# Kernel optimization log

Measured on AMD Instinct MI355X. Metric: run time of the kernel, lower is better.

The kernel has to match this reference:

```python
import jax, jax.numpy as jnp
import numpy as np

N1, N2 = 25000, 25000
N = N1 + N2
E = 800000
D1, D2 = 2000, 500
P = 128        # proj_dim
H, C = 4, 32   # heads, hidden_channels (H*C == 128)
NEG_SLOPE = 0.2


def glorot(key, shape):
    fan_in, fan_out = shape[0], shape[-1]
    s = jnp.sqrt(6.0 / (fan_in + fan_out))
    return jax.random.uniform(key, shape, jnp.float32, -s, s)


def setup_inputs() -> dict:
    key = jax.random.key(0)
    ks = jax.random.split(key, 12)
    return {
        "x_mrna": jax.random.normal(ks[0], (N1, D1), jnp.float32),
        "x_mirna": jax.random.normal(ks[1], (N2, D2), jnp.float32),
        "Wp1": glorot(ks[2], (D1, P)),
        "bp1": jnp.zeros((P,), jnp.float32),
        "Wp2": glorot(ks[3], (D2, P)),
        "bp2": jnp.zeros((P,), jnp.float32),
        "Wl": glorot(ks[4], (P, H * C)),   # GATv2 lin_l (source)
        "Wr": glorot(ks[5], (P, H * C)),   # GATv2 lin_r (target)
        "att": glorot(ks[6], (H, C)),       # GATv2 attention vector a
        "b_gat": jnp.zeros((H * C,), jnp.float32),
        "edge_index": jax.random.randint(ks[7], (2, E), 0, N, jnp.int32),
    }


def gatv2_conv(x, edge_index, Wl, Wr, att, b_gat):
    # x: [N, P] -> out: [N, H*C]; PyG GATv2Conv, add_self_loops=False, concat=True
    src, dst = edge_index[0], edge_index[1]
    xl = (x @ Wl).reshape(N, H, C)  # source-side transform
    xr = (x @ Wr).reshape(N, H, C)  # target-side transform
    # per-edge attention logits: a . LeakyReLU(xl[src] + xr[dst])  -> [E, H]
    g = jax.nn.leaky_relu(xl[src] + xr[dst], NEG_SLOPE)
    e = jnp.einsum('ehc,hc->eh', g, att)
    # softmax over incoming edges per destination node, per head
    m = jax.ops.segment_max(e, dst, num_segments=N)          # [N, H]
    ex = jnp.exp(e - m[dst])                                  # [E, H]
    denom = jax.ops.segment_sum(ex, dst, num_segments=N)     # [N, H]
    alpha = ex / (denom[dst] + 1e-16)                         # [E, H]
    msg = alpha[:, :, None] * xl[src]                         # [E, H, C]
    out = jax.ops.segment_sum(msg, dst, num_segments=N)      # [N, H, C]
    return out.reshape(N, H * C) + b_gat


def reference(x_mrna, x_mirna, Wp1, bp1, Wp2, bp2, Wl, Wr, att, b_gat, edge_index):
    # per-omic projection to shared proj_dim, then stack into one node set
    h1 = x_mrna @ Wp1 + bp1
    h2 = x_mirna @ Wp2 + bp2
    x = jnp.concatenate([h1, h2], axis=0)  # [N, P]
    out = gatv2_conv(x, edge_index, Wl, Wr, att, b_gat)
    return jax.nn.elu(out)
```

## Files before the change

### kernel.cpp

```cpp
#include <hip/hip_runtime.h>

#define NN 50000
#define NE 800000
#define PD 128
#define NBLK 196
#define GB1 391
#define M_HALF 25000

typedef __attribute__((ext_vector_type(8))) short bf16x8;
typedef __attribute__((ext_vector_type(4))) float f32x4;

__device__ __forceinline__ float bf2f(unsigned short h) {
  union { unsigned u; float f; } v; v.u = ((unsigned)h) << 16; return v.f;
}
__device__ __forceinline__ unsigned short f2bf(float f) {
  union { float f; unsigned u; } v; v.f = f;
  unsigned r = (v.u + 0x7FFFu + ((v.u >> 16) & 1u)) >> 16;
  return (unsigned short)r;
}
__device__ __forceinline__ unsigned pack2(float a, float b) {
  return (unsigned)f2bf(a) | ((unsigned)f2bf(b) << 16);
}

__global__ __launch_bounds__(256) void wtrans(
    const float* __restrict__ Wp1, const float* __restrict__ Wp2,
    const float* __restrict__ Wl, const float* __restrict__ Wr,
    const float* __restrict__ bp1, const float* __restrict__ bp2,
    unsigned short* __restrict__ Wct1, unsigned short* __restrict__ Wct2,
    float* __restrict__ biasc) {
  int b = blockIdx.x, n = threadIdx.x;
  __shared__ float arow[128];
  const float* W = (n < 128) ? Wl : Wr;
  int nc = n & 127;
  if (b < 2560) {
    int is1 = (b < 2048) ? 1 : 0;
    int k = is1 ? b : (b - 2048);
    int Kv = is1 ? 2000 : 500;
    unsigned short v = 0;
    if (k < Kv) {
      if (n < 128) arow[n] = is1 ? Wp1[k * 128 + n] : Wp2[k * 128 + n];
      __syncthreads();
      float s = 0.f;
      for (int p = 0; p < 128; ++p) s += arow[p] * W[p * 128 + nc];
      v = f2bf(s);
    }
    int ch = k >> 5, kq = (k >> 3) & 3, e = k & 7;
    size_t idx = (size_t)ch * 8192 + (size_t)(n * 4 + (kq ^ ((n >> 1) & 3))) * 8 + e;
    if (is1) Wct1[idx] = v; else Wct2[idx] = v;
  } else {
    float s1 = 0.f, s2 = 0.f;
    for (int p = 0; p < 128; ++p) {
      float w = W[p * 128 + nc];
      s1 += bp1[p] * w;
      s2 += bp2[p] * w;
    }
    biasc[n] = s1;
    biasc[256 + n] = s2;
  }
}

__global__ __launch_bounds__(256) void big_gemm(
    const float* __restrict__ x1, const float* __restrict__ x2,
    const unsigned short* __restrict__ Wct1, const unsigned short* __restrict__ Wct2,
    const float* __restrict__ biasc,
    unsigned short* __restrict__ XLb, float* __restrict__ XR) {
  __shared__ __align__(64) unsigned short lds[2 * 10752];
  int tid = threadIdx.x;
  int wave = tid >> 6, lane = tid & 63;
  int m16 = lane & 15, quad = lane >> 4;

  int inp = (blockIdx.x >= GB1) ? 1 : 0;
  int blk = inp ? (blockIdx.x - GB1) : blockIdx.x;
  const float* A = inp ? x2 : x1;
  const unsigned short* Wct = inp ? Wct2 : Wct1;
  const int K = inp ? 500 : 2000;
  const int nch = inp ? 16 : 63;
  int row0 = blk * 64;

  int ar = tid >> 2, ako = (tid & 3) << 3;
  bool arow_ok = (row0 + ar) < M_HALF;
  const float* aptr = A + (size_t)(row0 + ar) * K + ako;

  int swz = (quad ^ ((m16 >> 1) & 3)) << 3;
  int boffA[4], boffB[4];
#pragma unroll
  for (int i = 0; i < 4; ++i) boffA[i] = (i * 16 + m16) * 40 + quad * 8;
#pragma unroll
  for (int j = 0; j < 4; ++j) boffB[j] = (wave * 64 + j * 16 + m16) * 32 + swz;

  f32x4 acc[4][4];
#pragma unroll
  for (int i = 0; i < 4; ++i)
#pragma unroll
    for (int j = 0; j < 4; ++j) acc[i][j] = (f32x4){0.f, 0.f, 0.f, 0.f};

  float4 pa0, pa1;

#define GLB(ch, buf)                                                          \
  {                                                                           \
    const unsigned short* wp_ = Wct + (size_t)(ch) * 8192;                    \
    unsigned short* bb_ = lds + (buf) * 10752 + 2560;                         \
    _Pragma("unroll") for (int ii = 0; ii < 4; ++ii) {                        \
      int gb_ = (ii * 4 + wave) * 64;                                         \
      __builtin_amdgcn_global_load_lds(                                       \
          (const __attribute__((address_space(1))) void*)(wp_ +               \
              (size_t)(gb_ + lane) * 8),                                      \
          (__attribute__((address_space(3))) void*)(bb_ + (size_t)gb_ * 8),   \
          16, 0, 0);                                                          \
    }                                                                         \
  }

#define LOADA(ch)                                                             \
  {                                                                           \
    int k0_ = (ch) * 32;                                                      \
    if (arow_ok) {                                                            \
      pa0 = *(const float4*)(aptr + k0_);                                     \
      pa1 = *(const float4*)(aptr + k0_ + 4);                                 \
    }                                                                         \
  }

#define STOREA(buf)                                                           \
  {                                                                           \
    unsigned short* As_ = lds + (buf) * 10752;                                \
    uint4 wA;                                                                 \
    if (arow_ok) {                                                            \
      wA.x = pack2(pa0.x, pa0.y); wA.y = pack2(pa0.z, pa0.w);                 \
      wA.z = pack2(pa1.x, pa1.y); wA.w = pack2(pa1.z, pa1.w);                 \
    } else { wA.x = wA.y = wA.z = wA.w = 0u; }                                \
    *(uint4*)(As_ + ar * 40 + ako) = wA;                                      \
  }

  GLB(0, 0);
  LOADA(0);
  STOREA(0);
  __syncthreads();

  for (int ch = 0; ch < nch; ++ch) {
    int cur = ch & 1;
    if (ch + 1 < nch) { GLB(ch + 1, cur ^ 1); LOADA(ch + 1); }
    {
      const unsigned short* As_ = lds + cur * 10752;
      const unsigned short* Bs_ = As_ + 2560;
      bf16x8 a[4], b[4];
#pragma unroll
      for (int i = 0; i < 4; ++i) a[i] = *(const bf16x8*)(As_ + boffA[i]);
#pragma unroll
      for (int j = 0; j < 4; ++j) b[j] = *(const bf16x8*)(Bs_ + boffB[j]);
#pragma unroll
      for (int i = 0; i < 4; ++i)
#pragma unroll
        for (int j = 0; j < 4; ++j)
          acc[i][j] =
              __builtin_amdgcn_mfma_f32_16x16x32_bf16(a[i], b[j], acc[i][j], 0, 0, 0);
    }
    if (ch + 1 < nch) STOREA(cur ^ 1);
    __syncthreads();
  }

  const float* bc = biasc + inp * 256;
#pragma unroll
  for (int i = 0; i < 4; ++i) {
    int rb = row0 + i * 16 + quad * 4;
#pragma unroll
    for (int j = 0; j < 4; ++j) {
      int c = wave * 64 + j * 16 + m16;
      float bv = bc[c];
#pragma unroll
      for (int r = 0; r < 4; ++r) {
        if (rb + r < M_HALF) {
          size_t grow = (size_t)inp * M_HALF + rb + r;
          float v = acc[i][j][r] + bv;
          if (c < PD) XLb[grow * PD + c] = f2bf(v);
          else XR[grow * PD + (c - PD)] = v;
        }
      }
    }
  }
#undef GLB
#undef LOADA
#undef STOREA
}

__global__ __launch_bounds__(256) void zero_deg(int* __restrict__ deg) {
  int i = blockIdx.x * 256 + threadIdx.x;
  if (i < NN) deg[i] = 0;
}

__global__ __launch_bounds__(256) void hist(const int* __restrict__ edge,
                                            int* __restrict__ deg) {
  int i = blockIdx.x * 256 + threadIdx.x;
  if (i < NE) atomicAdd(&deg[edge[NE + i]], 1);
}

__global__ __launch_bounds__(256) void scan1(const int* __restrict__ deg,
                                             int* __restrict__ bsum) {
  __shared__ int sd[256];
  int i = blockIdx.x * 256 + threadIdx.x;
  sd[threadIdx.x] = (i < NN) ? deg[i] : 0;
  __syncthreads();
  for (int off = 128; off > 0; off >>= 1) {
    if (threadIdx.x < off) sd[threadIdx.x] += sd[threadIdx.x + off];
    __syncthreads();
  }
  if (threadIdx.x == 0) bsum[blockIdx.x] = sd[0];
}

__global__ __launch_bounds__(64) void scan2(const int* __restrict__ bsum,
                                            int* __restrict__ boff) {
  if (threadIdx.x == 0) {
    int run = 0;
    for (int b = 0; b < NBLK; ++b) { boff[b] = run; run += bsum[b]; }
  }
}

__global__ __launch_bounds__(256) void scan3(const int* __restrict__ deg,
                                             const int* __restrict__ boff,
                                             int* __restrict__ start,
                                             int* __restrict__ cursor) {
  __shared__ int sd[256];
  int i = blockIdx.x * 256 + threadIdx.x;
  int v = (i < NN) ? deg[i] : 0;
  sd[threadIdx.x] = v;
  __syncthreads();
  for (int off = 1; off < 256; off <<= 1) {
    int t = (threadIdx.x >= off) ? sd[threadIdx.x - off] : 0;
    __syncthreads();
    sd[threadIdx.x] += t;
    __syncthreads();
  }
  if (i < NN) {
    int excl = boff[blockIdx.x] + sd[threadIdx.x] - v;
    start[i] = excl;
    cursor[i] = excl;
  }
  if (blockIdx.x == 0 && threadIdx.x == 0) start[NN] = NE;
}

__global__ __launch_bounds__(256) void scatter(const int* __restrict__ edge,
                                               int* __restrict__ cursor,
                                               int* __restrict__ esrc) {
  int i = blockIdx.x * 256 + threadIdx.x;
  if (i < NE) {
    int dst = edge[NE + i];
    int pos = atomicAdd(&cursor[dst], 1);
    esrc[pos] = edge[i];
  }
}

__global__ __launch_bounds__(256) void gat_fused(
    const unsigned short* __restrict__ XLb, const float* __restrict__ XR,
    const float* __restrict__ att, const float* __restrict__ bg,
    const int* __restrict__ start, const int* __restrict__ esrc,
    float* __restrict__ out) {
  int wave = threadIdx.x >> 6, lane = threadIdx.x & 63;
  int d = blockIdx.x * 4 + wave;
  int f0 = lane * 2;

  float2 xr = *(const float2*)(XR + (size_t)d * PD + f0);
  float a0c = att[f0], a1c = att[f0 + 1];

  int s = start[d], e_end = start[d + 1];

  float m = -INFINITY, l = 0.f, acc0 = 0.f, acc1 = 0.f;
  for (int j = s; j < e_end; ++j) {
    int src = esrc[j];
    unsigned xlu = *(const unsigned*)(XLb + (size_t)src * PD + f0);
    float xl0 = bf2f((unsigned short)(xlu & 0xFFFFu));
    float xl1 = bf2f((unsigned short)(xlu >> 16));
    float z0 = xl0 + xr.x, z1 = xl1 + xr.y;
    float g0 = z0 > 0.f ? z0 : 0.2f * z0;
    float g1 = z1 > 0.f ? z1 : 0.2f * z1;
    float t = a0c * g0 + a1c * g1;
    t += __shfl_xor(t, 1);
    t += __shfl_xor(t, 2);
    t += __shfl_xor(t, 4);
    t += __shfl_xor(t, 8);
    float mn = fmaxf(m, t);
    float c = __expf(m - mn);
    float p = __expf(t - mn);
    l = l * c + p;
    acc0 = acc0 * c + p * xl0;
    acc1 = acc1 * c + p * xl1;
    m = mn;
  }

  float inv = 1.f / (l + 1e-16f);
  float v0 = acc0 * inv + bg[f0];
  float v1 = acc1 * inv + bg[f0 + 1];
  v0 = v0 > 0.f ? v0 : expm1f(v0);
  v1 = v1 > 0.f ? v1 : expm1f(v1);
  *(float2*)(out + (size_t)d * PD + f0) = make_float2(v0, v1);
}

extern "C" void kernel_launch(void* const* d_in, const int* in_sizes, int n_in,
                              void* d_out, int out_size, void* d_ws, size_t ws_size,
                              hipStream_t stream) {
  const float* x1  = (const float*)d_in[0];
  const float* x2  = (const float*)d_in[1];
  const float* Wp1 = (const float*)d_in[2];
  const float* bp1 = (const float*)d_in[3];
  const float* Wp2 = (const float*)d_in[4];
  const float* bp2 = (const float*)d_in[5];
  const float* Wl  = (const float*)d_in[6];
  const float* Wr  = (const float*)d_in[7];
  const float* att = (const float*)d_in[8];
  const float* bg  = (const float*)d_in[9];
  const int*   edge = (const int*)d_in[10];

  char* ws = (char*)d_ws;
  unsigned short* XLb   = (unsigned short*)(ws);
  float*          XR    = (float*)(ws + 12800000);
  int*            esrc  = (int*)(ws + 38400000);
  int*            start = (int*)(ws + 41600000);
  int*            cursor = (int*)(ws + 41800192);
  int*            deg   = (int*)(ws + 42000384);
  int*            bsum  = (int*)(ws + 42200576);
  int*            boff  = (int*)(ws + 42201600);
  unsigned short* Wct1  = (unsigned short*)(ws + 42202624);
  unsigned short* Wct2  = (unsigned short*)(ws + 43251200);
  float*          biasc = (float*)(ws + 43513344);

  wtrans<<<2561, 256, 0, stream>>>(Wp1, Wp2, Wl, Wr, bp1, bp2, Wct1, Wct2, biasc);

  zero_deg<<<NBLK, 256, 0, stream>>>(deg);
  hist<<<(NE + 255) / 256, 256, 0, stream>>>(edge, deg);
  scan1<<<NBLK, 256, 0, stream>>>(deg, bsum);
  scan2<<<1, 64, 0, stream>>>(bsum, boff);
  scan3<<<NBLK, 256, 0, stream>>>(deg, boff, start, cursor);
  scatter<<<(NE + 255) / 256, 256, 0, stream>>>(edge, cursor, esrc);

  big_gemm<<<GB1 * 2, 256, 0, stream>>>(x1, x2, Wct1, Wct2, biasc, XLb, XR);

  gat_fused<<<NN / 4, 256, 0, stream>>>(XLb, XR, att, bg, start, esrc,
                                        (float*)d_out);
}
```

Before: 579.7 us.

## Pipeline GEMM loads with manual waitcnts, merge small kernels, unroll GAT edge loop

The GEMM main loop now prefetches A two chunks ahead and replaces __syncthreads with explicit lgkmcnt/vmcnt waits plus a raw barrier and sched_barriers, so global loads overlap the MFMA work. Out-of-range rows are clamped to row 0 instead of branching. The degree zeroing is folded into the weight-transform launch, and the serial scan2 kernel is removed by having each scan3 block reduce the preceding block sums itself. The GAT aggregation loop is unrolled by four so four gathered XL loads are in flight at once. The hand-written wait counts carry a correctness risk if the number of outstanding loads does not match the assumed value.

```diff
diff --git a/kernel.cpp b/kernel.cpp
--- a/kernel.cpp
+++ b/kernel.cpp
@@ -27,9 +27,14 @@
     const float* __restrict__ Wl, const float* __restrict__ Wr,
     const float* __restrict__ bp1, const float* __restrict__ bp2,
     unsigned short* __restrict__ Wct1, unsigned short* __restrict__ Wct2,
-    float* __restrict__ biasc) {
+    float* __restrict__ biasc, int* __restrict__ deg) {
   int b = blockIdx.x, n = threadIdx.x;
   __shared__ float arow[128];
+  if (b > 2560) {
+    int i = (b - 2561) * 256 + n;
+    if (i < NN) deg[i] = 0;
+    return;
+  }
   const float* W = (n < 128) ? Wl : Wr;
   int nc = n & 127;
   if (b < 2560) {
@@ -78,8 +83,9 @@
   int row0 = blk * 64;
 
   int ar = tid >> 2, ako = (tid & 3) << 3;
-  bool arow_ok = (row0 + ar) < M_HALF;
-  const float* aptr = A + (size_t)(row0 + ar) * K + ako;
+  int arc = row0 + ar;
+  bool arow_ok = arc < M_HALF;
+  const float* aptr = A + (size_t)(arow_ok ? arc : 0) * K + ako;
 
   int swz = (quad ^ ((m16 >> 1) & 3)) << 3;
   int boffA[4], boffB[4];
@@ -101,7 +107,7 @@
     const unsigned short* wp_ = Wct + (size_t)(ch) * 8192;                    \
     unsigned short* bb_ = lds + (buf) * 10752 + 2560;                         \
     _Pragma("unroll") for (int ii = 0; ii < 4; ++ii) {                        \
-      int gb_ = (ii * 4 + wave) * 64;                                         \
+      int gb_ = wave * 256 + ii * 64;                                         \
       __builtin_amdgcn_global_load_lds(                                       \
           (const __attribute__((address_space(1))) void*)(wp_ +               \
               (size_t)(gb_ + lane) * 8),                                      \
@@ -113,10 +119,8 @@
 #define LOADA(ch)                                                             \
   {                                                                           \
     int k0_ = (ch) * 32;                                                      \
-    if (arow_ok) {                                                            \
-      pa0 = *(const float4*)(aptr + k0_);                                     \
-      pa1 = *(const float4*)(aptr + k0_ + 4);                                 \
-    }                                                                         \
+    pa0 = *(const float4*)(aptr + k0_);                                       \
+    pa1 = *(const float4*)(aptr + k0_ + 4);                                   \
   }
 
 #define STOREA(buf)                                                           \
@@ -130,14 +134,24 @@
     *(uint4*)(As_ + ar * 40 + ako) = wA;                                      \
   }
 
+  LOADA(0);
   GLB(0, 0);
-  LOADA(0);
   STOREA(0);
-  __syncthreads();
+  LOADA(1);
 
   for (int ch = 0; ch < nch; ++ch) {
     int cur = ch & 1;
-    if (ch + 1 < nch) { GLB(ch + 1, cur ^ 1); LOADA(ch + 1); }
+    asm volatile("s_waitcnt lgkmcnt(0)" ::: "memory");
+    __builtin_amdgcn_s_barrier();
+    __builtin_amdgcn_sched_barrier(0);
+    if (ch + 1 < nch) {
+      GLB(ch + 1, cur ^ 1);
+      __builtin_amdgcn_sched_barrier(0);
+      asm volatile("s_waitcnt vmcnt(6)" ::: "memory");
+    } else {
+      asm volatile("s_waitcnt vmcnt(0)" ::: "memory");
+    }
+    __builtin_amdgcn_sched_barrier(0);
     {
       const unsigned short* As_ = lds + cur * 10752;
       const unsigned short* Bs_ = As_ + 2560;
@@ -153,8 +167,10 @@
           acc[i][j] =
               __builtin_amdgcn_mfma_f32_16x16x32_bf16(a[i], b[j], acc[i][j], 0, 0, 0);
     }
-    if (ch + 1 < nch) STOREA(cur ^ 1);
-    __syncthreads();
+    if (ch + 1 < nch) {
+      STOREA(cur ^ 1);
+      if (ch + 2 < nch) LOADA(ch + 2);
+    }
   }
 
   const float* bc = biasc + inp * 256;
@@ -179,11 +195,6 @@
 #undef GLB
 #undef LOADA
 #undef STOREA
-}
-
-__global__ __launch_bounds__(256) void zero_deg(int* __restrict__ deg) {
-  int i = blockIdx.x * 256 + threadIdx.x;
-  if (i < NN) deg[i] = 0;
 }
 
 __global__ __launch_bounds__(256) void hist(const int* __restrict__ edge,
@@ -205,35 +216,34 @@
   if (threadIdx.x == 0) bsum[blockIdx.x] = sd[0];
 }
 
-__global__ __launch_bounds__(64) void scan2(const int* __restrict__ bsum,
-                                            int* __restrict__ boff) {
-  if (threadIdx.x == 0) {
-    int run = 0;
-    for (int b = 0; b < NBLK; ++b) { boff[b] = run; run += bsum[b]; }
-  }
-}
-
 __global__ __launch_bounds__(256) void scan3(const int* __restrict__ deg,
-                                             const int* __restrict__ boff,
+                                             const int* __restrict__ bsum,
                                              int* __restrict__ start,
                                              int* __restrict__ cursor) {
   __shared__ int sd[256];
-  int i = blockIdx.x * 256 + threadIdx.x;
+  __shared__ int sb[256];
+  int t = threadIdx.x;
+  int i = blockIdx.x * 256 + t;
+  sb[t] = (t < blockIdx.x) ? bsum[t] : 0;
   int v = (i < NN) ? deg[i] : 0;
-  sd[threadIdx.x] = v;
+  sd[t] = v;
   __syncthreads();
+  for (int off = 128; off > 0; off >>= 1) {
+    if (t < off) sb[t] += sb[t + off];
+    __syncthreads();
+  }
   for (int off = 1; off < 256; off <<= 1) {
-    int t = (threadIdx.x >= off) ? sd[threadIdx.x - off] : 0;
+    int x = (t >= off) ? sd[t - off] : 0;
     __syncthreads();
-    sd[threadIdx.x] += t;
+    sd[t] += x;
     __syncthreads();
   }
   if (i < NN) {
-    int excl = boff[blockIdx.x] + sd[threadIdx.x] - v;
+    int excl = sb[0] + sd[t] - v;
     start[i] = excl;
     cursor[i] = excl;
   }
-  if (blockIdx.x == 0 && threadIdx.x == 0) start[NN] = NE;
+  if (blockIdx.x == 0 && t == 0) start[NN] = NE;
 }
 
 __global__ __launch_bounds__(256) void scatter(const int* __restrict__ edge,
@@ -262,27 +272,43 @@
   int s = start[d], e_end = start[d + 1];
 
   float m = -INFINITY, l = 0.f, acc0 = 0.f, acc1 = 0.f;
-  for (int j = s; j < e_end; ++j) {
-    int src = esrc[j];
-    unsigned xlu = *(const unsigned*)(XLb + (size_t)src * PD + f0);
-    float xl0 = bf2f((unsigned short)(xlu & 0xFFFFu));
-    float xl1 = bf2f((unsigned short)(xlu >> 16));
-    float z0 = xl0 + xr.x, z1 = xl1 + xr.y;
-    float g0 = z0 > 0.f ? z0 : 0.2f * z0;
-    float g1 = z1 > 0.f ? z1 : 0.2f * z1;
-    float t = a0c * g0 + a1c * g1;
-    t += __shfl_xor(t, 1);
-    t += __shfl_xor(t, 2);
-    t += __shfl_xor(t, 4);
-    t += __shfl_xor(t, 8);
-    float mn = fmaxf(m, t);
-    float c = __expf(m - mn);
-    float p = __expf(t - mn);
-    l = l * c + p;
-    acc0 = acc0 * c + p * xl0;
-    acc1 = acc1 * c + p * xl1;
-    m = mn;
-  }
+
+#define UPD(xlu)                                                              \
+  {                                                                           \
+    float xl0 = bf2f((unsigned short)((xlu) & 0xFFFFu));                      \
+    float xl1 = bf2f((unsigned short)((xlu) >> 16));                          \
+    float z0 = xl0 + xr.x, z1 = xl1 + xr.y;                                   \
+    float g0 = z0 > 0.f ? z0 : 0.2f * z0;                                     \
+    float g1 = z1 > 0.f ? z1 : 0.2f * z1;                                     \
+    float t = a0c * g0 + a1c * g1;                                            \
+    t += __shfl_xor(t, 1);                                                    \
+    t += __shfl_xor(t, 2);                                                    \
+    t += __shfl_xor(t, 4);                                                    \
+    t += __shfl_xor(t, 8);                                                    \
+    float mn = fmaxf(m, t);                                                   \
+    float c = __expf(m - mn);                                                 \
+    float p = __expf(t - mn);                                                 \
+    l = l * c + p;                                                            \
+    acc0 = acc0 * c + p * xl0;                                                \
+    acc1 = acc1 * c + p * xl1;                                                \
+    m = mn;                                                                   \
+  }
+
+  int j = s;
+  for (; j + 4 <= e_end; j += 4) {
+    int s0 = esrc[j], s1 = esrc[j + 1], s2 = esrc[j + 2], s3 = esrc[j + 3];
+    unsigned u0 = *(const unsigned*)(XLb + (size_t)s0 * PD + f0);
+    unsigned u1 = *(const unsigned*)(XLb + (size_t)s1 * PD + f0);
+    unsigned u2 = *(const unsigned*)(XLb + (size_t)s2 * PD + f0);
+    unsigned u3 = *(const unsigned*)(XLb + (size_t)s3 * PD + f0);
+    UPD(u0); UPD(u1); UPD(u2); UPD(u3);
+  }
+  for (; j < e_end; ++j) {
+    int s0 = esrc[j];
+    unsigned u0 = *(const unsigned*)(XLb + (size_t)s0 * PD + f0);
+    UPD(u0);
+  }
+#undef UPD
 
   float inv = 1.f / (l + 1e-16f);
   float v0 = acc0 * inv + bg[f0];
@@ -315,18 +341,16 @@
   int*            cursor = (int*)(ws + 41800192);
   int*            deg   = (int*)(ws + 42000384);
   int*            bsum  = (int*)(ws + 42200576);
-  int*            boff  = (int*)(ws + 42201600);
   unsigned short* Wct1  = (unsigned short*)(ws + 42202624);
   unsigned short* Wct2  = (unsigned short*)(ws + 43251200);
   float*          biasc = (float*)(ws + 43513344);
 
-  wtrans<<<2561, 256, 0, stream>>>(Wp1, Wp2, Wl, Wr, bp1, bp2, Wct1, Wct2, biasc);
-
-  zero_deg<<<NBLK, 256, 0, stream>>>(deg);
+  wtrans<<<2757, 256, 0, stream>>>(Wp1, Wp2, Wl, Wr, bp1, bp2, Wct1, Wct2,
+                                   biasc, deg);
+
   hist<<<(NE + 255) / 256, 256, 0, stream>>>(edge, deg);
   scan1<<<NBLK, 256, 0, stream>>>(deg, bsum);
-  scan2<<<1, 64, 0, stream>>>(bsum, boff);
-  scan3<<<NBLK, 256, 0, stream>>>(deg, boff, start, cursor);
+  scan3<<<NBLK, 256, 0, stream>>>(deg, bsum, start, cursor);
   scatter<<<(NE + 255) / 256, 256, 0, stream>>>(edge, cursor, esrc);
 
   big_gemm<<<GB1 * 2, 256, 0, stream>>>(x1, x2, Wct1, Wct2, biasc, XLb, XR);
```

After: 531.0 us. 1.09x faster.
